# Optimization experiments

Measured on AMD Instinct MI355X. Metric: run time of the kernel, lower is better.

Reference implementation:

```python
import jax, jax.numpy as jnp
import numpy as np
import math

B, S, E, H = 2, 2048, 1024, 16
D = E // H  # head_dim = 64


def setup_inputs() -> dict:
    key = jax.random.key(0)
    ks = jax.random.split(key, 12)
    scale = 1.0 / math.sqrt(E)
    inp = {
        "q": jax.random.normal(ks[0], (B, S, E), jnp.float32),
        "k": jax.random.normal(ks[1], (B, S, E), jnp.float32),
        "v": jax.random.normal(ks[2], (B, S, E), jnp.float32),
        # causal mask, broadcast over batch and heads
        "mask": jnp.tril(jnp.ones((S, S), jnp.bool_))[None, None, :, :],
        "Wq": jax.random.normal(ks[3], (E, E), jnp.float32) * scale,
        "bq": jnp.zeros((E,), jnp.float32),
        "Wk": jax.random.normal(ks[4], (E, E), jnp.float32) * scale,
        "bk": jnp.zeros((E,), jnp.float32),
        "Wv": jax.random.normal(ks[5], (E, E), jnp.float32) * scale,
        "bv": jnp.zeros((E,), jnp.float32),
        "Wo": jax.random.normal(ks[6], (E, E), jnp.float32) * scale,
        "bo": jnp.zeros((E,), jnp.float32),
    }
    return inp


def _heads(x, W, b):
    # nn.Linear: x @ W.T + b, then split into heads -> [B, H, S, D]
    y = x @ W.T + b
    return y.reshape(B, S, H, D).transpose(0, 2, 1, 3)


def reference(q, k, v, mask, Wq, bq, Wk, bk, Wv, bv, Wo, bo):
    qh = _heads(q, Wq, bq)   # [B,H,S,D]
    kh = _heads(k, Wk, bk)
    vh = _heads(v, Wv, bv)
    scores = jnp.einsum("bhqd,bhkd->bhqk", qh, kh) / math.sqrt(D)
    scores = jnp.where(mask, scores, -1e9)
    probs = jax.nn.softmax(scores, axis=-1)  # dropout is identity in eval
    ctx = jnp.einsum("bhqk,bhkd->bhqd", probs, vh)
    ctx = ctx.transpose(0, 2, 1, 3).reshape(B, S, E)
    return ctx @ Wo.T + bo
```

## Files before the change

kernel.cpp:

```cpp
#include <hip/hip_runtime.h>
#include <hip/hip_bf16.h>
#include <cstdint>

#define PB 2
#define PS 2048
#define PE 1024
#define PH 16
#define PD 64

typedef __attribute__((ext_vector_type(8))) short short8;
typedef __attribute__((ext_vector_type(8))) ushort u16x8;
typedef __attribute__((ext_vector_type(4))) float f32x4;

static __device__ __forceinline__ float bf2f(ushort u) {
  return __uint_as_float(((unsigned)u) << 16);
}
static __device__ __forceinline__ ushort f2bf(float f) {
  unsigned u = __float_as_uint(f);
  u += 0x7fffu + ((u >> 16) & 1u);
  return (ushort)(u >> 16);
}
static __device__ __forceinline__ unsigned pkbf(float a, float b) {
  __hip_bfloat162 h = __float22bfloat162_rn(make_float2(a, b));
  return *reinterpret_cast<unsigned*>(&h);
}
static __device__ __forceinline__ u16x8 cvt8(f32x4 a, f32x4 b) {
  union { unsigned u[4]; u16x8 v; } r;
  r.u[0] = pkbf(a[0], a[1]); r.u[1] = pkbf(a[2], a[3]);
  r.u[2] = pkbf(b[0], b[1]); r.u[3] = pkbf(b[2], b[3]);
  return r.v;
}

static __device__ __forceinline__ void async16(void* lds, const void* g) {
  __attribute__((address_space(3))) unsigned* l =
      reinterpret_cast<__attribute__((address_space(3))) unsigned*>(
          reinterpret_cast<uintptr_t>(lds));
  const __attribute__((address_space(1))) unsigned* gp =
      reinterpret_cast<const __attribute__((address_space(1))) unsigned*>(
          reinterpret_cast<uintptr_t>(g));
  __builtin_amdgcn_global_load_lds(gp, l, 16, 0, 0);
}

__global__ __launch_bounds__(256)
void cvt_kernel(const float* __restrict__ s0, const float* __restrict__ s1,
                const float* __restrict__ s2, const float* __restrict__ s3,
                const float* __restrict__ s4, const float* __restrict__ s5,
                const float* __restrict__ s6,
                ushort* d0, ushort* d1, ushort* d2, ushort* d3, ushort* d4,
                ushort* d5, ushort* d6) {
  const int t = blockIdx.y;
  const float* src = t == 0 ? s0 : t == 1 ? s1 : t == 2 ? s2 : t == 3 ? s3
                   : t == 4 ? s4 : t == 5 ? s5 : s6;
  ushort* dst = t == 0 ? d0 : t == 1 ? d1 : t == 2 ? d2 : t == 3 ? d3
              : t == 4 ? d4 : t == 5 ? d5 : d6;
  const size_t n = (t < 3) ? (size_t)4194304 : (size_t)1048576;
  const size_t i0 = ((size_t)blockIdx.x * 256 + threadIdx.x) * 16;
  if (i0 >= n) return;
  const f32x4 a = *(const f32x4*)(src + i0);
  const f32x4 b = *(const f32x4*)(src + i0 + 4);
  const f32x4 c = *(const f32x4*)(src + i0 + 8);
  const f32x4 d = *(const f32x4*)(src + i0 + 12);
  *(u16x8*)(dst + i0) = cvt8(a, b);
  *(u16x8*)(dst + i0 + 8) = cvt8(c, d);
}

template <bool SWAP>
__device__ __forceinline__ void gemm_core(const ushort* __restrict__ A,
                                          const ushort* __restrict__ W,
                                          int m0, int n0,
                                          ushort* As, ushort* Bs,
                                          f32x4 acc[4][4]) {
  const int tid  = threadIdx.x;
  const int wave = tid >> 6;
  const int lane = tid & 63;
  const int quad = lane >> 4;
  const int lrow = lane & 15;
  const int wm = wave >> 1;
  const int wn = wave & 1;
  const int row0 = tid >> 2;
  const int kc8  = (tid & 3) * 8;

  for (int kt = 0; kt < PE; kt += 32) {
    async16(As + (size_t)wave * 512,        A + (size_t)(m0 + row0)      * PE + kt + kc8);
    async16(As + 2048 + (size_t)wave * 512, A + (size_t)(m0 + row0 + 64) * PE + kt + kc8);
    async16(Bs + (size_t)wave * 512,        W + (size_t)(n0 + row0)      * PE + kt + kc8);
    async16(Bs + 2048 + (size_t)wave * 512, W + (size_t)(n0 + row0 + 64) * PE + kt + kc8);
    __syncthreads();
    short8 af[4], bf[4];
#pragma unroll
    for (int i = 0; i < 4; ++i) {
      af[i] = *(const short8*)(As + (wm * 64 + i * 16 + lrow) * 32 + quad * 8);
      bf[i] = *(const short8*)(Bs + (wn * 64 + i * 16 + lrow) * 32 + quad * 8);
    }
#pragma unroll
    for (int i = 0; i < 4; ++i)
#pragma unroll
      for (int j = 0; j < 4; ++j) {
        if (SWAP)
          acc[i][j] = __builtin_amdgcn_mfma_f32_16x16x32_bf16(bf[j], af[i], acc[i][j], 0, 0, 0);
        else
          acc[i][j] = __builtin_amdgcn_mfma_f32_16x16x32_bf16(af[i], bf[j], acc[i][j], 0, 0, 0);
      }
    __syncthreads();
  }
}

__global__ __launch_bounds__(256)
void qkv_kernel(const ushort* __restrict__ q, const ushort* __restrict__ k,
                const ushort* __restrict__ v,
                const ushort* __restrict__ Wq, const ushort* __restrict__ Wk,
                const ushort* __restrict__ Wv,
                const float* __restrict__ bq, const float* __restrict__ bk,
                const float* __restrict__ bv,
                ushort* __restrict__ qh, ushort* __restrict__ kh,
                ushort* __restrict__ vt) {
  __shared__ __align__(16) ushort As[128 * 32];
  __shared__ __align__(16) ushort Bs[128 * 32];
  const int which = blockIdx.y >> 3;
  const int n0 = (blockIdx.y & 7) * 128;
  const int m0 = blockIdx.x * 128;
  const ushort* A  = which == 0 ? q  : (which == 1 ? k  : v);
  const ushort* W  = which == 0 ? Wq : (which == 1 ? Wk : Wv);
  const float* bi  = which == 0 ? bq : (which == 1 ? bk : bv);

  const int lane = threadIdx.x & 63;
  const int wave = threadIdx.x >> 6;
  const int quad = lane >> 4, lrow = lane & 15;
  const int wm = wave >> 1, wn = wave & 1;

  f32x4 acc[4][4] = {};
  if (which == 2) {
    gemm_core<true>(A, W, m0, n0, As, Bs, acc);
#pragma unroll
    for (int j = 0; j < 4; ++j) {
#pragma unroll
      for (int i = 0; i < 4; ++i) {
        const int xrow = m0 + wm * 64 + i * 16 + lrow;
        const int b = xrow >> 11, s = xrow & 2047;
#pragma unroll
        for (int r = 0; r < 4; ++r) {
          const int dcol = n0 + wn * 64 + j * 16 + quad * 4 + r;
          const int h = dcol >> 6, d = dcol & 63;
          vt[((size_t)((b << 4) + h) << 17) + ((size_t)d << 11) + s] =
              f2bf(acc[i][j][r] + bi[dcol]);
        }
      }
    }
  } else {
    gemm_core<false>(A, W, m0, n0, As, Bs, acc);
    ushort* Out = which == 0 ? qh : kh;
#pragma unroll
    for (int j = 0; j < 4; ++j) {
      const int col = n0 + wn * 64 + j * 16 + lrow;
      const float bias = bi[col];
      const int h = col >> 6, d = col & 63;
#pragma unroll
      for (int i = 0; i < 4; ++i)
#pragma unroll
        for (int r = 0; r < 4; ++r) {
          const int row = m0 + wm * 64 + i * 16 + quad * 4 + r;
          const int b = row >> 11, s = row & 2047;
          Out[((size_t)((b << 4) + h) << 17) + ((size_t)s << 6) + d] =
              f2bf(acc[i][j][r] + bias);
        }
    }
  }
}

__global__ __launch_bounds__(256)
void outproj_kernel(const ushort* __restrict__ ctx, const ushort* __restrict__ Wo,
                    const float* __restrict__ bo, float* __restrict__ out) {
  __shared__ __align__(16) ushort As[128 * 32];
  __shared__ __align__(16) ushort Bs[128 * 32];
  const int n0 = blockIdx.y * 128;
  const int m0 = blockIdx.x * 128;

  f32x4 acc[4][4] = {};
  gemm_core<false>(ctx, Wo, m0, n0, As, Bs, acc);

  const int lane = threadIdx.x & 63;
  const int wave = threadIdx.x >> 6;
  const int quad = lane >> 4, lrow = lane & 15;
  const int wm = wave >> 1, wn = wave & 1;
#pragma unroll
  for (int j = 0; j < 4; ++j) {
    const int col = n0 + wn * 64 + j * 16 + lrow;
    const float bias = bo[col];
#pragma unroll
    for (int i = 0; i < 4; ++i)
#pragma unroll
      for (int r = 0; r < 4; ++r) {
        const int row = m0 + wm * 64 + i * 16 + quad * 4 + r;
        out[((size_t)row << 10) + col] = acc[i][j][r] + bias;
      }
  }
}

#define SW_IDX(r, g) (((r) << 6) + ((((g) ^ ((r) & 7))) << 3))
#define QSCALE 0.180336879f
#define SOFF 24.0f

__global__ __launch_bounds__(256)
void attn_kernel(const ushort* __restrict__ qh, const ushort* __restrict__ kh,
                 const ushort* __restrict__ vt, ushort* __restrict__ ctx) {
  __shared__ __align__(16) ushort Ks[2][4096];
  __shared__ __align__(16) ushort Vs[2][4096];
  __shared__ __align__(16) ushort Ps[4][1024];
  const int tid  = threadIdx.x;
  const int wave = tid >> 6;
  const int lane = tid & 63;
  const int quad = lane >> 4;
  const int lrow = lane & 15;
  const int bh = blockIdx.x, b = bh >> 4, h = bh & 15;
  const size_t base = (size_t)bh << 17;
  const int srow = tid >> 2;
  const int sg0  = (tid & 3) * 2;
  const int pr   = wave * 16 + lrow;
  ushort* Pw = &Ps[wave][0];
  const int prow = lrow << 6;

  const int qb = 31 - blockIdx.y;
  const int q0 = qb * 64;

  short8 qf0, qf1;
  {
    const ushort* qp = qh + base + (size_t)(q0 + pr) * 64 + quad * 8;
    const u16x8 a = *(const u16x8*)qp;
    const u16x8 c = *(const u16x8*)(qp + 32);
#pragma unroll
    for (int j = 0; j < 8; ++j) {
      qf0[j] = (short)f2bf(bf2f(a[j]) * QSCALE);
      qf1[j] = (short)f2bf(bf2f(c[j]) * QSCALE);
    }
  }

  f32x4 o_acc[4] = {};
  float l_i = 0.f;

  u16x8 kst0, kst1, vst0, vst1;
  {
    const ushort* kp = kh + base + (size_t)srow * 64 + sg0 * 8;
    kst0 = *(const u16x8*)kp; kst1 = *(const u16x8*)(kp + 8);
    const ushort* vp = vt + base + (size_t)srow * 2048 + sg0 * 8;
    vst0 = *(const u16x8*)vp; vst1 = *(const u16x8*)(vp + 8);
  }

  for (int kt = 0; kt <= qb; ++kt) {
    const int buf = kt & 1;
    *(u16x8*)&Ks[buf][SW_IDX(srow, sg0)]     = kst0;
    *(u16x8*)&Ks[buf][SW_IDX(srow, sg0 + 1)] = kst1;
    *(u16x8*)&Vs[buf][SW_IDX(srow, sg0)]     = vst0;
    *(u16x8*)&Vs[buf][SW_IDX(srow, sg0 + 1)] = vst1;
    __syncthreads();

    if (kt < qb) {
      const ushort* kp = kh + base + (size_t)((kt + 1) * 64 + srow) * 64 + sg0 * 8;
      kst0 = *(const u16x8*)kp; kst1 = *(const u16x8*)(kp + 8);
      const ushort* vp = vt + base + (size_t)srow * 2048 + (kt + 1) * 64 + sg0 * 8;
      vst0 = *(const u16x8*)vp; vst1 = *(const u16x8*)(vp + 8);
    }

    f32x4 st[4] = {};
#pragma unroll
    for (int nt = 0; nt < 4; ++nt) {
      const int r = nt * 16 + lrow;
      const short8 kb0 = *(const short8*)&Ks[buf][SW_IDX(r, quad)];
      const short8 kb1 = *(const short8*)&Ks[buf][SW_IDX(r, quad + 4)];
      st[nt] = __builtin_amdgcn_mfma_f32_16x16x32_bf16(kb0, qf0, st[nt], 0, 0, 0);
      st[nt] = __builtin_amdgcn_mfma_f32_16x16x32_bf16(kb1, qf1, st[nt], 0, 0, 0);
    }

    if (kt == qb) {
#pragma unroll
      for (int nt = 0; nt < 4; ++nt)
#pragma unroll
        for (int r = 0; r < 4; ++r)
          if (nt * 16 + quad * 4 + r > pr) st[nt][r] = -1e30f;
    }

    float rs = 0.f;
#pragma unroll
    for (int nt = 0; nt < 4; ++nt) {
      float p0 = exp2f(st[nt][0] - SOFF);
      float p1 = exp2f(st[nt][1] - SOFF);
      float p2 = exp2f(st[nt][2] - SOFF);
      float p3 = exp2f(st[nt][3] - SOFF);
      rs += (p0 + p1) + (p2 + p3);
      uint2 pk;
      pk.x = pkbf(p0, p1); pk.y = pkbf(p2, p3);
      *(uint2*)&Pw[prow + (((nt * 2 + (quad >> 1)) ^ (lrow & 7)) << 3) +
                   (quad & 1) * 4] = pk;
    }
    rs += __shfl_xor(rs, 16);
    rs += __shfl_xor(rs, 32);
    l_i += rs;

    const short8 pa0 = *(const short8*)&Pw[prow + ((quad ^ (lrow & 7)) << 3)];
    const short8 pa1 = *(const short8*)&Pw[prow + (((quad + 4) ^ (lrow & 7)) << 3)];
#pragma unroll
    for (int nt = 0; nt < 4; ++nt) {
      const int r = nt * 16 + lrow;
      const short8 vb0 = *(const short8*)&Vs[buf][SW_IDX(r, quad)];
      const short8 vb1 = *(const short8*)&Vs[buf][SW_IDX(r, quad + 4)];
      o_acc[nt] = __builtin_amdgcn_mfma_f32_16x16x32_bf16(vb0, pa0, o_acc[nt], 0, 0, 0);
      o_acc[nt] = __builtin_amdgcn_mfma_f32_16x16x32_bf16(vb1, pa1, o_acc[nt], 0, 0, 0);
    }
  }

  const float inv = 1.f / l_i;
  const size_t rowb = ((size_t)b << 21) + ((size_t)(q0 + pr) << 10) + (h << 6);
#pragma unroll
  for (int nt = 0; nt < 4; ++nt) {
    uint2 u;
    u.x = pkbf(o_acc[nt][0] * inv, o_acc[nt][1] * inv);
    u.y = pkbf(o_acc[nt][2] * inv, o_acc[nt][3] * inv);
    *(uint2*)(ctx + rowb + nt * 16 + quad * 4) = u;
  }
}

extern "C" void kernel_launch(void* const* d_in, const int* in_sizes, int n_in,
                              void* d_out, int out_size, void* d_ws, size_t ws_size,
                              hipStream_t stream) {
  const float* q  = (const float*)d_in[0];
  const float* k  = (const float*)d_in[1];
  const float* v  = (const float*)d_in[2];
  const float* Wq = (const float*)d_in[4];
  const float* bq = (const float*)d_in[5];
  const float* Wk = (const float*)d_in[6];
  const float* bk = (const float*)d_in[7];
  const float* Wv = (const float*)d_in[8];
  const float* bv = (const float*)d_in[9];
  const float* Wo = (const float*)d_in[10];
  const float* bo = (const float*)d_in[11];

  const size_t NTOK = (size_t)PB * PS * PE;
  const size_t NW   = (size_t)PE * PE;
  ushort* qh  = (ushort*)d_ws;
  ushort* kh  = qh + NTOK;
  ushort* vt  = kh + NTOK;
  ushort* qc  = vt + NTOK;
  ushort* kc  = qc + NTOK;
  ushort* vc  = kc + NTOK;
  ushort* wqc = vc + NTOK;
  ushort* wkc = wqc + NW;
  ushort* wvc = wkc + NW;
  ushort* woc = wvc + NW;
  ushort* ctx = qc;

  cvt_kernel<<<dim3(1024, 7), dim3(256), 0, stream>>>(
      q, k, v, Wq, Wk, Wv, Wo, qc, kc, vc, wqc, wkc, wvc, woc);
  qkv_kernel<<<dim3(32, 24), dim3(256), 0, stream>>>(
      qc, kc, vc, wqc, wkc, wvc, bq, bk, bv, qh, kh, vt);
  attn_kernel<<<dim3(32, 32), dim3(256), 0, stream>>>(qh, kh, vt, ctx);
  outproj_kernel<<<dim3(32, 8), dim3(256), 0, stream>>>(
      ctx, woc, bo, (float*)d_out);
}
```

Before: 237.9 us.

## Double-buffer LDS tiles in projection GEMM core to overlap loads with MFMA

```diff
diff --git a/kernel.cpp b/kernel.cpp
--- a/kernel.cpp
+++ b/kernel.cpp
@@ -80,17 +80,28 @@
   const int row0 = tid >> 2;
   const int kc8  = (tid & 3) * 8;
 
+  auto stage = [&](int buf, int kt) {
+    ushort* Ab = As + buf * 4096;
+    ushort* Bb = Bs + buf * 4096;
+    async16(Ab + (size_t)wave * 512,        A + (size_t)(m0 + row0)      * PE + kt + kc8);
+    async16(Ab + 2048 + (size_t)wave * 512, A + (size_t)(m0 + row0 + 64) * PE + kt + kc8);
+    async16(Bb + (size_t)wave * 512,        W + (size_t)(n0 + row0)      * PE + kt + kc8);
+    async16(Bb + 2048 + (size_t)wave * 512, W + (size_t)(n0 + row0 + 64) * PE + kt + kc8);
+  };
+
+  stage(0, 0);
+  __syncthreads();
+  int cur = 0;
+
   for (int kt = 0; kt < PE; kt += 32) {
-    async16(As + (size_t)wave * 512,        A + (size_t)(m0 + row0)      * PE + kt + kc8);
-    async16(As + 2048 + (size_t)wave * 512, A + (size_t)(m0 + row0 + 64) * PE + kt + kc8);
-    async16(Bs + (size_t)wave * 512,        W + (size_t)(n0 + row0)      * PE + kt + kc8);
-    async16(Bs + 2048 + (size_t)wave * 512, W + (size_t)(n0 + row0 + 64) * PE + kt + kc8);
-    __syncthreads();
+    if (kt + 32 < PE) stage(cur ^ 1, kt + 32);
+    const ushort* Ab = As + cur * 4096;
+    const ushort* Bb = Bs + cur * 4096;
     short8 af[4], bf[4];
 #pragma unroll
     for (int i = 0; i < 4; ++i) {
-      af[i] = *(const short8*)(As + (wm * 64 + i * 16 + lrow) * 32 + quad * 8);
-      bf[i] = *(const short8*)(Bs + (wn * 64 + i * 16 + lrow) * 32 + quad * 8);
+      af[i] = *(const short8*)(Ab + (wm * 64 + i * 16 + lrow) * 32 + quad * 8);
+      bf[i] = *(const short8*)(Bb + (wn * 64 + i * 16 + lrow) * 32 + quad * 8);
     }
 #pragma unroll
     for (int i = 0; i < 4; ++i)
@@ -102,6 +113,7 @@
           acc[i][j] = __builtin_amdgcn_mfma_f32_16x16x32_bf16(af[i], bf[j], acc[i][j], 0, 0, 0);
       }
     __syncthreads();
+    cur ^= 1;
   }
 }
 
@@ -114,8 +126,8 @@
                 const float* __restrict__ bv,
                 ushort* __restrict__ qh, ushort* __restrict__ kh,
                 ushort* __restrict__ vt) {
-  __shared__ __align__(16) ushort As[128 * 32];
-  __shared__ __align__(16) ushort Bs[128 * 32];
+  __shared__ __align__(16) ushort As[2 * 128 * 32];
+  __shared__ __align__(16) ushort Bs[2 * 128 * 32];
   const int which = blockIdx.y >> 3;
   const int n0 = (blockIdx.y & 7) * 128;
   const int m0 = blockIdx.x * 128;
@@ -170,8 +182,8 @@
 __global__ __launch_bounds__(256)
 void outproj_kernel(const ushort* __restrict__ ctx, const ushort* __restrict__ Wo,
                     const float* __restrict__ bo, float* __restrict__ out) {
-  __shared__ __align__(16) ushort As[128 * 32];
-  __shared__ __align__(16) ushort Bs[128 * 32];
+  __shared__ __align__(16) ushort As[2 * 128 * 32];
+  __shared__ __align__(16) ushort Bs[2 * 128 * 32];
   const int n0 = blockIdx.y * 128;
   const int m0 = blockIdx.x * 128;
 
```

Result: faster. 221.5 us (-6.9%).
